# Kernel optimization log

Measured on AMD Instinct MI355X. Metric: run time of the kernel, lower is better.

## Reference

```python
import jax, jax.numpy as jnp
import numpy as np

N = 32768          # total nodes in batch (M graphs * N_agents)
E = N * 8          # edges (k_neighbors = 8)
DIN = 16           # node_obs_dim
DE = 8             # edge_dim (rel_pos 2 + one-hot 4 + dist 1 + payoff 1)
HE = 128           # embed_hidden_size
C = 64             # TransformerConv out_channels
H = 4              # heads (concat)
HC = H * C         # 256, final node embedding dim
EPS = 1e-5


def _ln(x, g, b):
    m = x.mean(-1, keepdims=True)
    v = ((x - m) ** 2).mean(-1, keepdims=True)
    return (x - m) * jax.lax.rsqrt(v + EPS) * g + b


def _seg_softmax(s, seg, n):
    # numerically stable softmax over edges grouped by destination node
    m = jax.ops.segment_max(s, seg, num_segments=n)
    e = jnp.exp(s - m[seg])
    z = jax.ops.segment_sum(e, seg, num_segments=n)
    return e / z[seg]


def setup_inputs() -> dict:
    key = jax.random.key(0)
    ks = jax.random.split(key, 40)

    def w(i, shape):
        return jax.random.normal(ks[i], shape, jnp.float32) * 0.05

    inp = {
        "x": jax.random.normal(ks[0], (N, DIN), jnp.float32),
        "edge_index": jax.random.randint(ks[1], (2, E), 0, N, dtype=jnp.int32),
        "edge_attr": jax.random.normal(ks[2], (E, DE), jnp.float32),
        # EmbedConv: lin1 + LN + one hidden Linear + LN (embed_layer_N=1)
        "e_W1": w(3, (DIN + DE, HE)), "e_b1": jnp.zeros((HE,), jnp.float32),
        "e_g1": jnp.ones((HE,), jnp.float32), "e_be1": jnp.zeros((HE,), jnp.float32),
        "e_W2": w(4, (HE, HE)), "e_b2": jnp.zeros((HE,), jnp.float32),
        "e_g2": jnp.ones((HE,), jnp.float32), "e_be2": jnp.zeros((HE,), jnp.float32),
    }
    # Two TransformerConv layers; layer0 in=HE, layer1 in=HC (concat heads)
    for l, din in enumerate([HE, HC]):
        base = 5 + l * 6
        inp[f"l{l}_Wq"] = w(base, (din, HC));     inp[f"l{l}_bq"] = jnp.zeros((HC,), jnp.float32)
        inp[f"l{l}_Wk"] = w(base + 1, (din, HC)); inp[f"l{l}_bk"] = jnp.zeros((HC,), jnp.float32)
        inp[f"l{l}_Wv"] = w(base + 2, (din, HC)); inp[f"l{l}_bv"] = jnp.zeros((HC,), jnp.float32)
        inp[f"l{l}_We"] = w(base + 3, (DE, HC))   # lin_edge has no bias in PyG
        inp[f"l{l}_Ws"] = w(base + 4, (din, HC)); inp[f"l{l}_bs"] = jnp.zeros((HC,), jnp.float32)
    return inp


def _tconv(h, edge_attr, src, dst, Wq, bq, Wk, bk, Wv, bv, We, Ws, bs):
    q = (h @ Wq + bq).reshape(N, H, C)
    k = (h @ Wk + bk).reshape(N, H, C)
    v = (h @ Wv + bv).reshape(N, H, C)
    e = (edge_attr @ We).reshape(E, H, C)
    ke = k[src] + e                      # [E,H,C]
    ve = v[src] + e                      # [E,H,C]
    s = (q[dst] * ke).sum(-1) / np.float32(np.sqrt(C))  # [E,H]
    a = _seg_softmax(s, dst, N)          # softmax over in-edges of each dst
    out = jax.ops.segment_sum(a[..., None] * ve, dst, num_segments=N)
    return out.reshape(N, HC) + h @ Ws + bs  # root_weight skip + bias


def reference(x, edge_attr, e_W1, e_b1, e_g1, e_be1, e_W2, e_b2, e_g2, e_be2,
              l0_Wq, l0_bq, l0_Wk, l0_bk, l0_Wv, l0_bv, l0_We, l0_Ws, l0_bs,
              l1_Wq, l1_bq, l1_Wk, l1_bk, l1_Wv, l1_bv, l1_We, l1_Ws, l1_bs,
              edge_index):
    src, dst = edge_index[0], edge_index[1]
    # EmbedConv: per-edge MLP on cat(x_j, edge_attr), scatter-add to dst
    m = jnp.concatenate([x[src], edge_attr], axis=1)    # [E, DIN+DE]
    m = _ln(jax.nn.relu(m @ e_W1 + e_b1), e_g1, e_be1)
    m = _ln(jax.nn.relu(m @ e_W2 + e_b2), e_g2, e_be2)
    h = jax.ops.segment_sum(m, dst, num_segments=N)      # [N, HE]
    # Two TransformerConv layers with ReLU activations
    h = jax.nn.relu(_tconv(h, edge_attr, src, dst, l0_Wq, l0_bq, l0_Wk, l0_bk,
                           l0_Wv, l0_bv, l0_We, l0_Ws, l0_bs))
    h = jax.nn.relu(_tconv(h, edge_attr, src, dst, l1_Wq, l1_bq, l1_Wk, l1_bk,
                           l1_Wv, l1_bv, l1_We, l1_Ws, l1_bs))
    return h  # graph_aggr == 'node': [N, HC]
```

## Files before the change

### kernel.cpp

```cpp
#include <hip/hip_runtime.h>
#include <hip/hip_bf16.h>

#define NN 32768
#define NE 262144

typedef unsigned short u16;
typedef unsigned int   u32;
typedef __bf16 bf16x8 __attribute__((ext_vector_type(8)));
typedef float  f32x16 __attribute__((ext_vector_type(16)));

__device__ __forceinline__ float bf2f(u16 u){ return __uint_as_float(((u32)u)<<16); }
__device__ __forceinline__ u16 f2bf(float f){ __hip_bfloat16 h = __float2bfloat16(f); return *(u16*)&h; }
__device__ __forceinline__ float4 ldbf4(const u16* p){
  ushort4 u = *(const ushort4*)p;
  return make_float4(bf2f(u.x), bf2f(u.y), bf2f(u.z), bf2f(u.w));
}
__device__ __forceinline__ void gload16(const void* g, void* l){
  __builtin_amdgcn_global_load_lds(
      (const __attribute__((address_space(1))) void*)g,
      (__attribute__((address_space(3))) void*)l, 16, 0, 0);
}

__global__ void k_deg(const int* __restrict__ ei, int* deg){
  int e = blockIdx.x*256 + threadIdx.x;
  if (e < NE) atomicAdd(&deg[ei[NE + e]], 1);
}

__global__ void k_scan1(const int* __restrict__ deg, int* __restrict__ rowptr, int* __restrict__ bsum){
  const int t = threadIdx.x, b = blockIdx.x;
  const int i = b*256 + t;
  const int ln = t & 63, wv = t >> 6;
  int v = deg[i];
  #pragma unroll
  for (int d = 1; d < 64; d <<= 1){
    int u = __shfl_up(v, d, 64);
    if (ln >= d) v += u;
  }
  __shared__ int wsum[4];
  if (ln == 63) wsum[wv] = v;
  __syncthreads();
  int p = 0;
  #pragma unroll
  for (int w = 0; w < 4; w++) if (w < wv) p += wsum[w];
  v += p;
  rowptr[i + 1] = v;
  if (t == 255) bsum[b] = v;
}

__global__ void k_scan2(const int* __restrict__ bsum, int* __restrict__ boff){
  const int t = threadIdx.x;
  const int ln = t & 63, wv = t >> 6;
  int own = bsum[t];
  int v = own;
  #pragma unroll
  for (int d = 1; d < 64; d <<= 1){
    int u = __shfl_up(v, d, 64);
    if (ln >= d) v += u;
  }
  __shared__ int wsum[2];
  if (ln == 63) wsum[wv] = v;
  __syncthreads();
  if (wv == 1) v += wsum[0];
  boff[t] = v - own;
}

__global__ void k_scan3(int* __restrict__ rowptr, const int* __restrict__ boff){
  const int t = threadIdx.x, b = blockIdx.x;
  rowptr[1 + b*256 + t] += boff[b];
  if (b == 0 && t == 0) rowptr[0] = 0;
}

__global__ void k_fill(const int* __restrict__ ei, const int* __restrict__ rowptr,
                       int* cursor, const float* __restrict__ ea,
                       int* __restrict__ csrc, float4* __restrict__ ea_csr){
  int e = blockIdx.x*256 + threadIdx.x;
  if (e < NE){
    int d = ei[NE + e];
    int p = rowptr[d] + atomicAdd(&cursor[d], 1);
    csrc[p] = ei[e];
    float4 a = *(const float4*)&ea[(size_t)e*8];
    float4 b = *(const float4*)&ea[(size_t)e*8 + 4];
    ea_csr[(size_t)p*2]     = a;
    ea_csr[(size_t)p*2 + 1] = b;
  }
}

__global__ void k_b2p(const float* __restrict__ W2, const float* __restrict__ be1,
                      const float* __restrict__ b2, float* __restrict__ b2p){
  int f = threadIdx.x;
  float a = b2[f];
  for (int k = 0; k < 128; k++) a += be1[k]*W2[k*128 + f];
  b2p[f] = a;
}

__global__ void k_eprep(const float* __restrict__ W1, const float* __restrict__ b1,
                        const float* __restrict__ W2, const float* __restrict__ g1,
                        const float* __restrict__ b2p, __bf16* __restrict__ Ecat){
  int i = blockIdx.x*256 + threadIdx.x;
  if (i >= 2816) return;
  bf16x8 v;
  if (i < 512){
    int r = i & 31, hh = (i>>5)&1, ks = (i>>6)&1, rt = i>>7;
    int feat = rt*32 + r, k0 = ks*16 + hh*8;
    #pragma unroll
    for (int j = 0; j < 8; j++){
      int k = k0 + j;
      float val = (k < 24) ? W1[k*128 + feat] : ((k == 24) ? b1[feat] : 0.f);
      v[j] = (__bf16)val;
    }
  } else {
    int m = i - 512;
    int r = m & 31, hh = (m>>5)&1, q = m>>6;
    int ks = q % 9, rt = q / 9;
    int feat = rt*32 + r, k0 = ks*16 + hh*8;
    #pragma unroll
    for (int j = 0; j < 8; j++){
      int k = k0 + j;
      float val = (k < 128) ? g1[k]*W2[k*128 + feat] : ((k == 128) ? b2p[feat] : 0.f);
      v[j] = (__bf16)val;
    }
  }
  *(bf16x8*)&Ecat[(size_t)i*8] = v;
}

struct WPtrs { const float* w[8]; const float* b[8]; };

__global__ void k_wprep(WPtrs wp, __bf16* __restrict__ W0cat, __bf16* __restrict__ W1cat,
                        float* __restrict__ bcat0, float* __restrict__ bcat1){
  int gid = blockIdx.x*256 + threadIdx.x;
  if (gid < 16384){
    int mat = gid >> 12, v = gid & 4095;
    int colm = v & 255, q = v >> 8;
    int k0 = (q>>1)*16 + (q&1)*8;
    const float* W = wp.w[mat];
    bf16x8 vec;
    #pragma unroll
    for (int j = 0; j < 8; j++) vec[j] = (__bf16)W[(size_t)(k0+j)*256 + colm];
    *(bf16x8*)&W0cat[((size_t)q*1024 + mat*256 + colm)*8] = vec;
  } else if (gid < 49152){
    int g = gid - 16384;
    int mat = g >> 13, v = g & 8191;
    int colm = v & 255, q = v >> 8;
    int k0 = (q>>1)*16 + (q&1)*8;
    const float* W = wp.w[4+mat];
    bf16x8 vec;
    #pragma unroll
    for (int j = 0; j < 8; j++) vec[j] = (__bf16)W[(size_t)(k0+j)*256 + colm];
    *(bf16x8*)&W1cat[((size_t)q*1024 + mat*256 + colm)*8] = vec;
  } else if (gid < 51200){
    int g = gid - 49152;
    if (g < 1024) bcat0[g] = wp.b[g>>8][g&255];
    else { int h = g-1024; bcat1[h] = wp.b[4 + (h>>8)][h&255]; }
  }
}

__global__ __launch_bounds__(256, 1) void k_embed(
    const float* __restrict__ x, const float4* __restrict__ ea_csr,
    const int* __restrict__ csrc, const int* __restrict__ rowptr,
    const __bf16* __restrict__ Ecat,
    const float* __restrict__ g2, const float* __restrict__ be2,
    u16* __restrict__ h0b)
{
  __shared__ alignas(16) __bf16 sE[2816*8];
  __shared__ float sg2[128], sbe2[128];
  const int t = threadIdx.x;
  const int wv = t >> 6, ln = t & 63, hi = ln >> 5, c32 = ln & 31;

  #pragma unroll
  for (int k = 0; k < 11; k++){
    int base = k*256 + wv*64;
    gload16(Ecat + (size_t)(base + ln)*8, &sE[(size_t)base*8]);
  }
  if (t < 128){ sg2[t] = g2[t]; sbe2[t] = be2[t]; }
  asm volatile("s_waitcnt vmcnt(0)" ::: "memory");
  __syncthreads();

  const int d   = (blockIdx.x*4 + wv)*32 + c32;
  const int rp  = rowptr[d];
  const int deg = rowptr[d+1] - rp;
  int md = deg;
  #pragma unroll
  for (int m = 1; m < 32; m <<= 1) md = max(md, __shfl_xor(md, m, 32));

  f32x16 hacc[4] = {};

  bool vc = deg > 0;
  int p0 = vc ? rp : 0;
  int sc = csrc[p0];
  float4 xa = *(const float4*)&x[(size_t)sc*16 + hi*8];
  float4 xb = *(const float4*)&x[(size_t)sc*16 + hi*8 + 4];
  float4 ga = ea_csr[(size_t)p0*2];
  float4 gb = ea_csr[(size_t)p0*2 + 1];

  for (int j = 0; j < md; j++){
    const float vm = vc ? 1.f : 0.f;
    bf16x8 b1f0, b1f1;
    {
      float xv[8]; *(float4*)&xv[0] = xa; *(float4*)&xv[4] = xb;
      #pragma unroll
      for (int q = 0; q < 8; q++) b1f0[q] = (__bf16)(xv[q]*vm);
      float evv[8]; *(float4*)&evv[0] = ga; *(float4*)&evv[4] = gb;
      #pragma unroll
      for (int q = 0; q < 8; q++)
        b1f1[q] = (__bf16)(hi ? ((q == 0) ? vm : 0.f) : evv[q]*vm);
    }

    bool vn = (j + 1) < deg;
    int pn = vn ? (rp + j + 1) : 0;
    int sn = csrc[pn];
    float4 xan = *(const float4*)&x[(size_t)sn*16 + hi*8];
    float4 xbn = *(const float4*)&x[(size_t)sn*16 + hi*8 + 4];
    float4 gan = ea_csr[(size_t)pn*2];
    float4 gbn = ea_csr[(size_t)pn*2 + 1];

    f32x16 a1[4] = {};
    #pragma unroll
    for (int ks = 0; ks < 2; ks++)
      #pragma unroll
      for (int rt = 0; rt < 4; rt++){
        bf16x8 af = *(const bf16x8*)&sE[((((rt*2 + ks)*2 + hi)*32) + c32)*8];
        a1[rt] = __builtin_amdgcn_mfma_f32_32x32x16_bf16(af, ks ? b1f1 : b1f0, a1[rt], 0, 0, 0);
      }

    {
      float s1 = 0.f, s2 = 0.f;
      #pragma unroll
      for (int rt = 0; rt < 4; rt++)
        #pragma unroll
        for (int rg = 0; rg < 16; rg++){
          float v = fmaxf(a1[rt][rg], 0.f);
          a1[rt][rg] = v; s1 += v; s2 += v*v;
        }
      s1 += __shfl_xor(s1, 32, 64);
      s2 += __shfl_xor(s2, 32, 64);
      float mean = s1*(1.f/128.f);
      float rs = rsqrtf(s2*(1.f/128.f) - mean*mean + 1e-5f);
      #pragma unroll
      for (int rt = 0; rt < 4; rt++)
        #pragma unroll
        for (int rg = 0; rg < 16; rg++)
          a1[rt][rg] = (a1[rt][rg] - mean)*rs;
    }

    f32x16 a2[4] = {};
    #pragma unroll
    for (int ks = 0; ks < 8; ks++){
      const int tt = ks >> 1, bb = (ks & 1)*8;
      float snd[4], rcv[4];
      #pragma unroll
      for (int q = 0; q < 4; q++)
        snd[q] = hi ? a1[tt][bb + q] : a1[tt][bb + 4 + q];
      #pragma unroll
      for (int q = 0; q < 4; q++)
        rcv[q] = __shfl_xor(snd[q], 32, 64);
      bf16x8 bf;
      #pragma unroll
      for (int q = 0; q < 4; q++){
        float lo = hi ? rcv[q] : a1[tt][bb + q];
        float hh = hi ? a1[tt][bb + 4 + q] : rcv[q];
        bf[q]     = (__bf16)lo;
        bf[4 + q] = (__bf16)hh;
      }
      #pragma unroll
      for (int rt = 0; rt < 4; rt++){
        bf16x8 af = *(const bf16x8*)&sE[(512 + (((rt*9 + ks)*2 + hi)*32) + c32)*8];
        a2[rt] = __builtin_amdgcn_mfma_f32_32x32x16_bf16(af, bf, a2[rt], 0, 0, 0);
      }
    }
    {
      bf16x8 bf;
      #pragma unroll
      for (int q = 0; q < 8; q++)
        bf[q] = (__bf16)((!hi && q == 0) ? vm : 0.f);
      #pragma unroll
      for (int rt = 0; rt < 4; rt++){
        bf16x8 af = *(const bf16x8*)&sE[(512 + (((rt*9 + 8)*2 + hi)*32) + c32)*8];
        a2[rt] = __builtin_amdgcn_mfma_f32_32x32x16_bf16(af, bf, a2[rt], 0, 0, 0);
      }
    }

    {
      float s1 = 0.f, s2 = 0.f;
      #pragma unroll
      for (int rt = 0; rt < 4; rt++)
        #pragma unroll
        for (int rg = 0; rg < 16; rg++){
          float v = fmaxf(a2[rt][rg], 0.f);
          a2[rt][rg] = v; s1 += v; s2 += v*v;
        }
      s1 += __shfl_xor(s1, 32, 64);
      s2 += __shfl_xor(s2, 32, 64);
      float mean = s1*(1.f/128.f);
      float rs = rsqrtf(s2*(1.f/128.f) - mean*mean + 1e-5f);
      #pragma unroll
      for (int rt = 0; rt < 4; rt++)
        #pragma unroll
        for (int rg = 0; rg < 16; rg++)
          hacc[rt][rg] += (a2[rt][rg] - mean)*rs;
    }

    vc = vn;
    xa = xan; xb = xbn; ga = gan; gb = gbn;
  }

  const float dd = (float)deg;
  #pragma unroll
  for (int rt = 0; rt < 4; rt++)
    #pragma unroll
    for (int q = 0; q < 4; q++){
      int fb = rt*32 + 8*q + 4*hi;
      ushort4 o;
      o.x = f2bf(sg2[fb+0]*hacc[rt][q*4+0] + dd*sbe2[fb+0]);
      o.y = f2bf(sg2[fb+1]*hacc[rt][q*4+1] + dd*sbe2[fb+1]);
      o.z = f2bf(sg2[fb+2]*hacc[rt][q*4+2] + dd*sbe2[fb+2]);
      o.w = f2bf(sg2[fb+3]*hacc[rt][q*4+3] + dd*sbe2[fb+3]);
      *(ushort4*)&h0b[(size_t)d*128 + fb] = o;
    }
}

template<int K>
__global__ __launch_bounds__(256) void k_qkvs2(const u16* __restrict__ A,
    const __bf16* __restrict__ Wcat, const float* __restrict__ bcat,
    u16* __restrict__ qo, u16* __restrict__ ko, u16* __restrict__ vo, u16* __restrict__ so)
{
  __shared__ alignas(16) __bf16 sA[1024*8];
  __shared__ alignas(16) __bf16 sB[1024*8];
  const int t = threadIdx.x;
  const int swz = (blockIdx.x & 7)*256 + (blockIdx.x >> 3);
  const int r0 = (swz >> 3)*128, c0 = (swz & 7)*128;
  const int wv = t >> 6, ln = t & 63, hi = ln >> 5, c32 = ln & 31;
  const int wr = wv >> 1, wc = wv & 1;

  f32x16 acc[2][2] = {};
  for (int kc = 0; kc < K/64; kc++){
    __syncthreads();
    #pragma unroll
    for (int ii = 0; ii < 4; ii++){
      int v = ii*256 + wv*64 + ln;
      int r = v & 31, hh = (v>>5)&1, ks = (v>>6)&3, rt = v>>8;
      const u16* src = A + (size_t)(r0 + rt*32 + r)*K + kc*64 + ks*16 + hh*8;
      gload16(src, &sA[(size_t)(ii*256 + wv*64)*8]);
    }
    #pragma unroll
    for (int ii = 0; ii < 4; ii++){
      int v = ii*256 + wv*64 + ln;
      int col = v & 127, q = v >> 7;
      const __bf16* src = Wcat + ((size_t)(kc*8 + q)*1024 + c0 + col)*8;
      gload16(src, &sB[(size_t)(ii*256 + wv*64)*8]);
    }
    asm volatile("s_waitcnt vmcnt(0)" ::: "memory");
    __syncthreads();
    #pragma unroll
    for (int ks = 0; ks < 4; ks++){
      bf16x8 af0 = *(const bf16x8*)&sA[((((wr*2+0)*4 + ks)*2 + hi)*32 + c32)*8];
      bf16x8 af1 = *(const bf16x8*)&sA[((((wr*2+1)*4 + ks)*2 + hi)*32 + c32)*8];
      bf16x8 bf0 = *(const bf16x8*)&sB[(((ks*2 + hi)*128) + wc*64 + c32)*8];
      bf16x8 bf1 = *(const bf16x8*)&sB[(((ks*2 + hi)*128) + wc*64 + 32 + c32)*8];
      acc[0][0] = __builtin_amdgcn_mfma_f32_32x32x16_bf16(af0, bf0, acc[0][0], 0, 0, 0);
      acc[0][1] = __builtin_amdgcn_mfma_f32_32x32x16_bf16(af0, bf1, acc[0][1], 0, 0, 0);
      acc[1][0] = __builtin_amdgcn_mfma_f32_32x32x16_bf16(af1, bf0, acc[1][0], 0, 0, 0);
      acc[1][1] = __builtin_amdgcn_mfma_f32_32x32x16_bf16(af1, bf1, acc[1][1], 0, 0, 0);
    }
  }

  u16* om = (c0 < 256) ? qo : (c0 < 512) ? ko : (c0 < 768) ? vo : so;
  const int cb = c0 & 255;
  #pragma unroll
  for (int ci = 0; ci < 2; ci++){
    int colm = cb + wc*64 + ci*32 + c32;
    float bb = bcat[c0 + wc*64 + ci*32 + c32];
    #pragma unroll
    for (int ri = 0; ri < 2; ri++){
      #pragma unroll
      for (int rg = 0; rg < 16; rg++){
        int row = r0 + (wr*2 + ri)*32 + (rg&3) + 8*(rg>>2) + 4*hi;
        om[(size_t)row*256 + colm] = f2bf(acc[ri][ci][rg] + bb);
      }
    }
  }
}

template<bool OBF>
__global__ __launch_bounds__(256) void k_attn(
    const int* __restrict__ csrc, const int* __restrict__ rowptr,
    const float4* __restrict__ ea_csr, const float* __restrict__ We,
    const u16* __restrict__ qb, const u16* __restrict__ kb, const u16* __restrict__ vb,
    const u16* __restrict__ skb, void* __restrict__ outp)
{
  __shared__ float sWe[8*256];
  const int t = threadIdx.x;
  for (int i = t; i < 2048; i += 256) sWe[i] = We[i];
  __syncthreads();

  const float* eaf = (const float*)ea_csr;
  const int wv = t >> 6, ln = t & 63;
  const int f = (ln >> 4)*64 + (ln & 15)*4;
  const int iown = ln & 7;
  const int gbase = ln & ~15;
  const int gw = blockIdx.x*4 + wv, nW = gridDim.x*4;

#define ATT_PRE(KX, VX, EX, jj) do{                                        \
      int sj_ = ((jj) < 64) ? __shfl(sidx, (jj), 64) : csrc[rp + (jj)];    \
      KX = ldbf4(kb + (size_t)sj_*256 + f);                                \
      VX = ldbf4(vb + (size_t)sj_*256 + f);                                \
      EX = eaf[(size_t)(rp + (jj))*8 + iown];                              \
    }while(0)

#define ATT_STEP(KX, VX, EX) do{                                           \
      float spp = qv.x*KX.x + qv.y*KX.y + qv.z*KX.z + qv.w*KX.w;           \
      spp += EX*wqsel;                                                     \
      spp += __shfl_xor(spp, 1, 64); spp += __shfl_xor(spp, 2, 64);        \
      spp += __shfl_xor(spp, 4, 64); spp += __shfl_xor(spp, 8, 64);        \
      float nm = fmaxf(m, spp);                                            \
      float sc_ = __expf(m - nm);                                          \
      float pp = __expf(spp - nm);                                         \
      l = l*sc_ + pp;                                                      \
      o0 = o0*sc_ + pp*VX.x; o1 = o1*sc_ + pp*VX.y;                        \
      o2 = o2*sc_ + pp*VX.z; o3 = o3*sc_ + pp*VX.w;                        \
      weal = weal*sc_ + pp*EX;                                             \
      m = nm;                                                              \
    }while(0)

  for (int d = gw; d < NN; d += nW){
    const int rp = rowptr[d];
    const int dg = rowptr[d+1] - rp;
    float4 qv = ldbf4(qb + (size_t)d*256 + f);
    qv.x *= 0.125f; qv.y *= 0.125f; qv.z *= 0.125f; qv.w *= 0.125f;
    float4 sv = ldbf4(skb + (size_t)d*256 + f);

    float wqsel = 0.f;
    #pragma unroll
    for (int i = 0; i < 8; i++){
      float4 w = *(const float4*)&sWe[i*256 + f];
      float p = qv.x*w.x + qv.y*w.y + qv.z*w.z + qv.w*w.w;
      p += __shfl_xor(p, 1, 64); p += __shfl_xor(p, 2, 64);
      p += __shfl_xor(p, 4, 64); p += __shfl_xor(p, 8, 64);
      if ((ln & 15) == i) wqsel = p;
    }

    float m = -INFINITY, l = 0.f, o0 = 0, o1 = 0, o2 = 0, o3 = 0, weal = 0.f;

    if (dg > 0){
      int sidx = (ln < dg) ? csrc[rp + ln] : 0;
      float4 kA, vA, kB, vB; float eA, eB;
      ATT_PRE(kA, vA, eA, 0);
      if (dg > 1) ATT_PRE(kB, vB, eB, 1);

      int j = 0;
      while (j < dg){
        ATT_STEP(kA, vA, eA);
        if (j + 2 < dg) ATT_PRE(kA, vA, eA, j + 2);
        j++;
        if (j >= dg) break;
        ATT_STEP(kB, vB, eB);
        if (j + 2 < dg) ATT_PRE(kB, vB, eB, j + 2);
        j++;
      }
    }

    float il = (l > 0.f) ? 1.f/l : 0.f;
    float ec0 = 0, ec1 = 0, ec2 = 0, ec3 = 0;
    #pragma unroll
    for (int i = 0; i < 8; i++){
      float wi = __shfl(weal, gbase + i, 64);
      float4 w = *(const float4*)&sWe[i*256 + f];
      ec0 += wi*w.x; ec1 += wi*w.y; ec2 += wi*w.z; ec3 += wi*w.w;
    }
    o0 = fmaxf((o0 + ec0)*il + sv.x, 0.f);
    o1 = fmaxf((o1 + ec1)*il + sv.y, 0.f);
    o2 = fmaxf((o2 + ec2)*il + sv.z, 0.f);
    o3 = fmaxf((o3 + ec3)*il + sv.w, 0.f);
    if constexpr (OBF){
      ushort4 o; o.x = f2bf(o0); o.y = f2bf(o1); o.z = f2bf(o2); o.w = f2bf(o3);
      *(ushort4*)((u16*)outp + (size_t)d*256 + f) = o;
    } else {
      *(float4*)((float*)outp + (size_t)d*256 + f) = make_float4(o0, o1, o2, o3);
    }
  }
#undef ATT_PRE
#undef ATT_STEP
}

extern "C" void kernel_launch(void* const* d_in, const int* in_sizes, int n_in,
                              void* d_out, int out_size, void* d_ws, size_t ws_size,
                              hipStream_t stream)
{
  (void)in_sizes; (void)n_in; (void)out_size; (void)ws_size;
  const float* x   = (const float*)d_in[0];
  const int*   ei  = (const int*)  d_in[1];
  const float* ea  = (const float*)d_in[2];
  const float* eW1 = (const float*)d_in[3];
  const float* eb1 = (const float*)d_in[4];
  const float* eg1 = (const float*)d_in[5];
  const float* ebe1= (const float*)d_in[6];
  const float* eW2 = (const float*)d_in[7];
  const float* eb2 = (const float*)d_in[8];
  const float* eg2 = (const float*)d_in[9];
  const float* ebe2= (const float*)d_in[10];

  char* ws = (char*)d_ws;
  const size_t MB = (size_t)1 << 20;
  const size_t KB = (size_t)1 << 10;
  int*   deg    = (int*)(ws);
  int*   cursor = (int*)(ws + 128*KB);
  int*   rowptr = (int*)(ws + 256*KB);
  int*   bsum   = (int*)(ws + 400*KB);
  int*   boff   = (int*)(ws + 402*KB);
  float* b2p    = (float*)(ws + 404*KB);
  int*   csrc   = (int*)(ws + 1*MB);
  float4* ea_csr= (float4*)(ws + 4*MB);
  u16*   qb     = (u16*)(ws + 20*MB);
  u16*   kbuf   = (u16*)(ws + 36*MB);
  u16*   vbuf   = (u16*)(ws + 52*MB);
  u16*   skb    = (u16*)(ws + 68*MB);
  u16*   h1     = (u16*)(ws + 84*MB);
  u16*   h0b    = (u16*)(ws + 100*MB);
  __bf16* W0cat = (__bf16*)(ws + 108*MB);
  __bf16* W1cat = (__bf16*)(ws + 109*MB);
  float* bcat0  = (float*)(ws + 110*MB);
  float* bcat1  = (float*)(ws + 110*MB + 64*KB);
  __bf16* Ecat  = (__bf16*)(ws + 111*MB);

  hipMemsetAsync(deg, 0, 256*KB, stream);

  k_deg  <<<NE/256, 256, 0, stream>>>(ei, deg);
  k_scan1<<<128,    256, 0, stream>>>(deg, rowptr, bsum);
  k_scan2<<<1,      128, 0, stream>>>(bsum, boff);
  k_scan3<<<128,    256, 0, stream>>>(rowptr, boff);
  k_fill <<<NE/256, 256, 0, stream>>>(ei, rowptr, cursor, ea, csrc, ea_csr);
  k_b2p  <<<1,      128, 0, stream>>>(eW2, ebe1, eb2, b2p);
  k_eprep<<<11,     256, 0, stream>>>(eW1, eb1, eW2, eg1, b2p, Ecat);

  WPtrs wp;
  wp.w[0] = (const float*)d_in[11]; wp.b[0] = (const float*)d_in[12];
  wp.w[1] = (const float*)d_in[13]; wp.b[1] = (const float*)d_in[14];
  wp.w[2] = (const float*)d_in[15]; wp.b[2] = (const float*)d_in[16];
  wp.w[3] = (const float*)d_in[18]; wp.b[3] = (const float*)d_in[19];
  wp.w[4] = (const float*)d_in[20]; wp.b[4] = (const float*)d_in[21];
  wp.w[5] = (const float*)d_in[22]; wp.b[5] = (const float*)d_in[23];
  wp.w[6] = (const float*)d_in[24]; wp.b[6] = (const float*)d_in[25];
  wp.w[7] = (const float*)d_in[27]; wp.b[7] = (const float*)d_in[28];
  k_wprep<<<200, 256, 0, stream>>>(wp, W0cat, W1cat, bcat0, bcat1);

  k_embed<<<NN/128, 256, 0, stream>>>(x, ea_csr, csrc, rowptr, Ecat, eg2, ebe2, h0b);

  k_qkvs2<128><<<2048, 256, 0, stream>>>(h0b, W0cat, bcat0, qb, kbuf, vbuf, skb);
  k_attn<true><<<NN/4, 256, 0, stream>>>(csrc, rowptr, ea_csr, (const float*)d_in[17],
                                         qb, kbuf, vbuf, skb, (void*)h1);
  k_qkvs2<256><<<2048, 256, 0, stream>>>(h1, W1cat, bcat1, qb, kbuf, vbuf, skb);
  k_attn<false><<<NN/4, 256, 0, stream>>>(csrc, rowptr, ea_csr, (const float*)d_in[26],
                                          qb, kbuf, vbuf, skb, d_out);
}
```

Baseline: 336.8 us.

## Interleave K and V rows, double-buffer GEMM LDS, deepen attention prefetch

The QKV GEMM now writes K and V into one interleaved buffer (4 K values then 4 V values per lane chunk), so each gathered neighbor in the attention kernel is fetched with a single 16-byte load instead of two 8-byte loads from separate rows. The GEMM also double-buffers its LDS tiles, issuing the next K-chunk's global-to-LDS loads before computing the current one. The attention loop prefetches four neighbors ahead instead of two to hide gather latency. In exchange, the GEMM epilogue's scattered 2-byte stores become more strided, and LDS use and register pressure rise.

```diff
diff --git a/kernel.cpp b/kernel.cpp
--- a/kernel.cpp
+++ b/kernel.cpp
@@ -321,41 +321,48 @@
 template<int K>
 __global__ __launch_bounds__(256) void k_qkvs2(const u16* __restrict__ A,
     const __bf16* __restrict__ Wcat, const float* __restrict__ bcat,
-    u16* __restrict__ qo, u16* __restrict__ ko, u16* __restrict__ vo, u16* __restrict__ so)
+    u16* __restrict__ qo, u16* __restrict__ kvb, u16* __restrict__ so)
 {
-  __shared__ alignas(16) __bf16 sA[1024*8];
-  __shared__ alignas(16) __bf16 sB[1024*8];
+  __shared__ alignas(16) __bf16 sA[2][1024*8];
+  __shared__ alignas(16) __bf16 sB[2][1024*8];
   const int t = threadIdx.x;
   const int swz = (blockIdx.x & 7)*256 + (blockIdx.x >> 3);
   const int r0 = (swz >> 3)*128, c0 = (swz & 7)*128;
   const int wv = t >> 6, ln = t & 63, hi = ln >> 5, c32 = ln & 31;
   const int wr = wv >> 1, wc = wv & 1;
-
-  f32x16 acc[2][2] = {};
-  for (int kc = 0; kc < K/64; kc++){
-    __syncthreads();
+  const int NCH = K/64;
+
+  auto stage = [&](int kc, int b){
     #pragma unroll
     for (int ii = 0; ii < 4; ii++){
       int v = ii*256 + wv*64 + ln;
       int r = v & 31, hh = (v>>5)&1, ks = (v>>6)&3, rt = v>>8;
-      const u16* src = A + (size_t)(r0 + rt*32 + r)*K + kc*64 + ks*16 + hh*8;
-      gload16(src, &sA[(size_t)(ii*256 + wv*64)*8]);
+      gload16(A + (size_t)(r0 + rt*32 + r)*K + kc*64 + ks*16 + hh*8,
+              &sA[b][(size_t)(ii*256 + wv*64)*8]);
     }
     #pragma unroll
     for (int ii = 0; ii < 4; ii++){
       int v = ii*256 + wv*64 + ln;
       int col = v & 127, q = v >> 7;
-      const __bf16* src = Wcat + ((size_t)(kc*8 + q)*1024 + c0 + col)*8;
-      gload16(src, &sB[(size_t)(ii*256 + wv*64)*8]);
-    }
+      gload16(Wcat + ((size_t)(kc*8 + q)*1024 + c0 + col)*8,
+              &sB[b][(size_t)(ii*256 + wv*64)*8]);
+    }
+  };
+
+  stage(0, 0);
+  f32x16 acc[2][2] = {};
+  for (int kc = 0; kc < NCH; kc++){
     asm volatile("s_waitcnt vmcnt(0)" ::: "memory");
     __syncthreads();
+    if (kc + 1 < NCH) stage(kc + 1, (kc + 1) & 1);
+    const __bf16* cA = sA[kc & 1];
+    const __bf16* cB = sB[kc & 1];
     #pragma unroll
     for (int ks = 0; ks < 4; ks++){
-      bf16x8 af0 = *(const bf16x8*)&sA[((((wr*2+0)*4 + ks)*2 + hi)*32 + c32)*8];
-      bf16x8 af1 = *(const bf16x8*)&sA[((((wr*2+1)*4 + ks)*2 + hi)*32 + c32)*8];
-      bf16x8 bf0 = *(const bf16x8*)&sB[(((ks*2 + hi)*128) + wc*64 + c32)*8];
-      bf16x8 bf1 = *(const bf16x8*)&sB[(((ks*2 + hi)*128) + wc*64 + 32 + c32)*8];
+      bf16x8 af0 = *(const bf16x8*)&cA[((((wr*2+0)*4 + ks)*2 + hi)*32 + c32)*8];
+      bf16x8 af1 = *(const bf16x8*)&cA[((((wr*2+1)*4 + ks)*2 + hi)*32 + c32)*8];
+      bf16x8 bf0 = *(const bf16x8*)&cB[(((ks*2 + hi)*128) + wc*64 + c32)*8];
+      bf16x8 bf1 = *(const bf16x8*)&cB[(((ks*2 + hi)*128) + wc*64 + 32 + c32)*8];
       acc[0][0] = __builtin_amdgcn_mfma_f32_32x32x16_bf16(af0, bf0, acc[0][0], 0, 0, 0);
       acc[0][1] = __builtin_amdgcn_mfma_f32_32x32x16_bf16(af0, bf1, acc[0][1], 0, 0, 0);
       acc[1][0] = __builtin_amdgcn_mfma_f32_32x32x16_bf16(af1, bf0, acc[1][0], 0, 0, 0);
@@ -363,18 +370,23 @@
     }
   }
 
-  u16* om = (c0 < 256) ? qo : (c0 < 512) ? ko : (c0 < 768) ? vo : so;
+  u16* omp; int rstride; int vadd = -1;
+  if (c0 < 256)      { omp = qo;  rstride = 256; }
+  else if (c0 < 512) { omp = kvb; rstride = 512; vadd = 0; }
+  else if (c0 < 768) { omp = kvb; rstride = 512; vadd = 4; }
+  else               { omp = so;  rstride = 256; }
   const int cb = c0 & 255;
   #pragma unroll
   for (int ci = 0; ci < 2; ci++){
     int colm = cb + wc*64 + ci*32 + c32;
+    int coff = (vadd >= 0) ? (((colm >> 2) << 3) + vadd + (colm & 3)) : colm;
     float bb = bcat[c0 + wc*64 + ci*32 + c32];
     #pragma unroll
     for (int ri = 0; ri < 2; ri++){
       #pragma unroll
       for (int rg = 0; rg < 16; rg++){
         int row = r0 + (wr*2 + ri)*32 + (rg&3) + 8*(rg>>2) + 4*hi;
-        om[(size_t)row*256 + colm] = f2bf(acc[ri][ci][rg] + bb);
+        omp[(size_t)row*rstride + coff] = f2bf(acc[ri][ci][rg] + bb);
       }
     }
   }
@@ -384,7 +396,7 @@
 __global__ __launch_bounds__(256) void k_attn(
     const int* __restrict__ csrc, const int* __restrict__ rowptr,
     const float4* __restrict__ ea_csr, const float* __restrict__ We,
-    const u16* __restrict__ qb, const u16* __restrict__ kb, const u16* __restrict__ vb,
+    const u16* __restrict__ qb, const u16* __restrict__ kvb,
     const u16* __restrict__ skb, void* __restrict__ outp)
 {
   __shared__ float sWe[8*256];
@@ -395,28 +407,31 @@
   const float* eaf = (const float*)ea_csr;
   const int wv = t >> 6, ln = t & 63;
   const int f = (ln >> 4)*64 + (ln & 15)*4;
+  const int kvo = ((ln >> 4)*16 + (ln & 15))*8;
   const int iown = ln & 7;
   const int gbase = ln & ~15;
   const int gw = blockIdx.x*4 + wv, nW = gridDim.x*4;
 
-#define ATT_PRE(KX, VX, EX, jj) do{                                        \
+#define ATT_PRE(RX, EX, jj) do{                                            \
       int sj_ = ((jj) < 64) ? __shfl(sidx, (jj), 64) : csrc[rp + (jj)];    \
-      KX = ldbf4(kb + (size_t)sj_*256 + f);                                \
-      VX = ldbf4(vb + (size_t)sj_*256 + f);                                \
+      RX = *(const int4*)&kvb[(size_t)sj_*512 + kvo];                      \
       EX = eaf[(size_t)(rp + (jj))*8 + iown];                              \
     }while(0)
 
-#define ATT_STEP(KX, VX, EX) do{                                           \
-      float spp = qv.x*KX.x + qv.y*KX.y + qv.z*KX.z + qv.w*KX.w;           \
-      spp += EX*wqsel;                                                     \
+#define ATT_STEP(RX, EX) do{                                               \
+      float kx0 = bf2f((u16)(RX.x & 0xffff)), kx1 = bf2f((u16)(((u32)RX.x)>>16)); \
+      float kx2 = bf2f((u16)(RX.y & 0xffff)), kx3 = bf2f((u16)(((u32)RX.y)>>16)); \
+      float vx0 = bf2f((u16)(RX.z & 0xffff)), vx1 = bf2f((u16)(((u32)RX.z)>>16)); \
+      float vx2 = bf2f((u16)(RX.w & 0xffff)), vx3 = bf2f((u16)(((u32)RX.w)>>16)); \
+      float spp = qv.x*kx0 + qv.y*kx1 + qv.z*kx2 + qv.w*kx3 + EX*wqsel;    \
       spp += __shfl_xor(spp, 1, 64); spp += __shfl_xor(spp, 2, 64);        \
       spp += __shfl_xor(spp, 4, 64); spp += __shfl_xor(spp, 8, 64);        \
       float nm = fmaxf(m, spp);                                            \
       float sc_ = __expf(m - nm);                                          \
       float pp = __expf(spp - nm);                                         \
       l = l*sc_ + pp;                                                      \
-      o0 = o0*sc_ + pp*VX.x; o1 = o1*sc_ + pp*VX.y;                        \
-      o2 = o2*sc_ + pp*VX.z; o3 = o3*sc_ + pp*VX.w;                        \
+      o0 = o0*sc_ + pp*vx0; o1 = o1*sc_ + pp*vx1;                          \
+      o2 = o2*sc_ + pp*vx2; o3 = o3*sc_ + pp*vx3;                          \
       weal = weal*sc_ + pp*EX;                                             \
       m = nm;                                                              \
     }while(0)
@@ -442,19 +457,18 @@
 
     if (dg > 0){
       int sidx = (ln < dg) ? csrc[rp + ln] : 0;
-      float4 kA, vA, kB, vB; float eA, eB;
-      ATT_PRE(kA, vA, eA, 0);
-      if (dg > 1) ATT_PRE(kB, vB, eB, 1);
+      int4 rA, rB, rC, rD; float eA, eB, eC, eD;
+      ATT_PRE(rA, eA, 0);
+      if (dg > 1) ATT_PRE(rB, eB, 1);
+      if (dg > 2) ATT_PRE(rC, eC, 2);
+      if (dg > 3) ATT_PRE(rD, eD, 3);
 
       int j = 0;
       while (j < dg){
-        ATT_STEP(kA, vA, eA);
-        if (j + 2 < dg) ATT_PRE(kA, vA, eA, j + 2);
-        j++;
-        if (j >= dg) break;
-        ATT_STEP(kB, vB, eB);
-        if (j + 2 < dg) ATT_PRE(kB, vB, eB, j + 2);
-        j++;
+        ATT_STEP(rA, eA); if (j + 4 < dg) ATT_PRE(rA, eA, j + 4); if (++j >= dg) break;
+        ATT_STEP(rB, eB); if (j + 4 < dg) ATT_PRE(rB, eB, j + 4); if (++j >= dg) break;
+        ATT_STEP(rC, eC); if (j + 4 < dg) ATT_PRE(rC, eC, j + 4); if (++j >= dg) break;
+        ATT_STEP(rD, eD); if (j + 4 < dg) ATT_PRE(rD, eD, j + 4); ++j;
       }
     }
 
@@ -510,8 +524,7 @@
   int*   csrc   = (int*)(ws + 1*MB);
   float4* ea_csr= (float4*)(ws + 4*MB);
   u16*   qb     = (u16*)(ws + 20*MB);
-  u16*   kbuf   = (u16*)(ws + 36*MB);
-  u16*   vbuf   = (u16*)(ws + 52*MB);
+  u16*   kvb    = (u16*)(ws + 36*MB);
   u16*   skb    = (u16*)(ws + 68*MB);
   u16*   h1     = (u16*)(ws + 84*MB);
   u16*   h0b    = (u16*)(ws + 100*MB);
@@ -544,10 +557,10 @@
 
   k_embed<<<NN/128, 256, 0, stream>>>(x, ea_csr, csrc, rowptr, Ecat, eg2, ebe2, h0b);
 
-  k_qkvs2<128><<<2048, 256, 0, stream>>>(h0b, W0cat, bcat0, qb, kbuf, vbuf, skb);
+  k_qkvs2<128><<<2048, 256, 0, stream>>>(h0b, W0cat, bcat0, qb, kvb, skb);
   k_attn<true><<<NN/4, 256, 0, stream>>>(csrc, rowptr, ea_csr, (const float*)d_in[17],
-                                         qb, kbuf, vbuf, skb, (void*)h1);
-  k_qkvs2<256><<<2048, 256, 0, stream>>>(h1, W1cat, bcat1, qb, kbuf, vbuf, skb);
+                                         qb, kvb, skb, (void*)h1);
+  k_qkvs2<256><<<2048, 256, 0, stream>>>(h1, W1cat, bcat1, qb, kvb, skb);
   k_attn<false><<<NN/4, 256, 0, stream>>>(csrc, rowptr, ea_csr, (const float*)d_in[26],
-                                          qb, kbuf, vbuf, skb, d_out);
-}
+                                          qb, kvb, skb, d_out);
+}
```

New measurement: 335.5 us. Within noise of the previous version (-0.4%).
